# Performance work log

Measured on AMD Instinct MI355X. Metric: run time of the kernel, lower is better.

The kernel has to match this reference:

```python
import jax, jax.numpy as jnp
import numpy as np

V, J, NB, NP = 100000, 24, 10, 207
PARENT = np.array([-1, 0, 0, 0, 1, 2, 3, 4, 5, 6, 7, 8, 9, 9, 9, 12, 13, 14, 16, 17, 18, 19, 20, 21])


def setup_inputs() -> dict:
    key = jax.random.key(0)
    ks = jax.random.split(key, 9)
    return {
        "beta": jax.random.normal(ks[0], (NB,), jnp.float32),
        "pose": jax.random.normal(ks[1], (J, 3), jnp.float32),
        "trans": jax.random.normal(ks[2], (3,), jnp.float32),
        "shapedirs": jax.random.normal(ks[3], (V, 3, NB), jnp.float32),
        "v_template": jax.random.normal(ks[4], (V, 3), jnp.float32),
        "J_regressor": jax.random.uniform(ks[5], (J, V), jnp.float32),
        "posedirs": jax.random.normal(ks[6], (V, 3, NP), jnp.float32),
        "weights": jax.random.uniform(ks[7], (V, J), jnp.float32),
        "faces": jax.random.randint(ks[8], (200000, 3), 0, V, jnp.int32),
    }


def _rodrigues(r):
    # r: [N,3] axis-angle -> [N,3,3] rotation matrices
    theta = jnp.sqrt(jnp.sum(r * r, axis=1, keepdims=True)) + 1e-8  # [N,1]
    rh = r / theta
    c = jnp.cos(theta)[:, :, None]  # [N,1,1]
    s = jnp.sin(theta)[:, :, None]
    z = jnp.zeros_like(rh[:, 0])
    K = jnp.stack([z, -rh[:, 2], rh[:, 1],
                   rh[:, 2], z, -rh[:, 0],
                   -rh[:, 1], rh[:, 0], z], axis=1).reshape(-1, 3, 3)
    outer = rh[:, :, None] * rh[:, None, :]
    I = jnp.eye(3, dtype=r.dtype)
    return c * I + (1.0 - c) * outer + s * K


def _with_zeros(Rt):
    # [3,4] -> [4,4] homogeneous
    bottom = jnp.array([[0.0, 0.0, 0.0, 1.0]], dtype=Rt.dtype)
    return jnp.concatenate([Rt, bottom], axis=0)


def reference(beta, pose, trans, shapedirs, v_template, J_regressor, posedirs, weights, faces):
    # shape blending
    v_shaped = jnp.einsum('vdb,b->vd', shapedirs, beta) + v_template  # [V,3]
    Jts = J_regressor @ v_shaped  # [J,3]
    R = _rodrigues(pose)  # [J,3,3]
    # pose blending: lrotmin = (R[1:] - I).flatten(), length 207
    lrotmin = (R[1:] - jnp.eye(3, dtype=R.dtype)).reshape(-1)
    v_posed = v_shaped + jnp.einsum('vdp,p->vd', posedirs, lrotmin)
    # forward kinematics along the 24-joint chain
    G = [_with_zeros(jnp.concatenate([R[0], Jts[0][:, None]], axis=1))]
    for i in range(1, J):
        p = int(PARENT[i])
        loc = _with_zeros(jnp.concatenate([R[i], (Jts[i] - Jts[p])[:, None]], axis=1))
        G.append(G[p] @ loc)
    stacked = jnp.stack(G, axis=0)  # [J,4,4]
    Jh = jnp.concatenate([Jts, jnp.zeros((J, 1), dtype=Jts.dtype)], axis=1)  # [J,4]
    corr = stacked @ Jh[:, :, None]  # [J,4,1]
    A = stacked - jnp.concatenate([jnp.zeros((J, 4, 3), dtype=stacked.dtype), corr], axis=2)
    # LBS skinning
    T = jnp.einsum('vj,jab->vab', weights, A)  # [V,4,4]
    rest = jnp.concatenate([v_posed, jnp.ones((v_posed.shape[0], 1), dtype=v_posed.dtype)], axis=1)  # [V,4]
    v = jnp.einsum('vab,vb->va', T, rest)[:, :3]
    vertices = v + trans[None, :]
    return vertices, faces
```

## Files before the change

### kernel.cpp

```cpp
#include <hip/hip_runtime.h>

#define V_N 100000
#define J_N 24
#define NB_N 10
#define NP_N 207
#define FLAT_P 621
#define FACE_I 600000
#define CHUNKS 50
#define CHUNK_V 2000
#define K1_BLK 1172
#define F_BLK  587

__device__ __constant__ int PARENT_D[24] = {
    -1, 0, 0, 0, 1, 2, 3, 4, 5, 6, 7, 8, 9, 9, 9, 12, 13, 14, 16, 17, 18, 19, 20, 21
};

__device__ __forceinline__ float wave_sum64(float x) {
    float t;
    t = __int_as_float(__builtin_amdgcn_update_dpp(0, __float_as_int(x), 0x111, 0xf, 0xf, true)); x += t;
    t = __int_as_float(__builtin_amdgcn_update_dpp(0, __float_as_int(x), 0x112, 0xf, 0xf, true)); x += t;
    t = __int_as_float(__builtin_amdgcn_update_dpp(0, __float_as_int(x), 0x114, 0xf, 0xf, true)); x += t;
    t = __int_as_float(__builtin_amdgcn_update_dpp(0, __float_as_int(x), 0x118, 0xf, 0xf, true)); x += t;
    t = __int_as_float(__builtin_amdgcn_update_dpp(0, __float_as_int(x), 0x142, 0xa, 0xf, true)); x += t;
    t = __int_as_float(__builtin_amdgcn_update_dpp(0, __float_as_int(x), 0x143, 0xc, 0xf, true)); x += t;
    return __int_as_float(__builtin_amdgcn_readlane(__float_as_int(x), 63));
}

__global__ __launch_bounds__(256) void kA_shape_faces(const float* __restrict__ shapedirs,
                                                      const float* __restrict__ vtemp,
                                                      const float* __restrict__ beta,
                                                      float* __restrict__ vshaped,
                                                      const int4* __restrict__ faces4,
                                                      float* __restrict__ out) {
    int b = blockIdx.x;
    if (b < K1_BLK) {
        int i = b * 256 + threadIdx.x;
        if (i >= V_N * 3) return;
        const float2* sd2 = reinterpret_cast<const float2*>(shapedirs + (size_t)i * NB_N);
        float2 p0 = sd2[0], p1 = sd2[1], p2 = sd2[2], p3 = sd2[3], p4 = sd2[4];
        float acc = vtemp[i];
        acc += p0.x * beta[0] + p0.y * beta[1];
        acc += p1.x * beta[2] + p1.y * beta[3];
        acc += p2.x * beta[4] + p2.y * beta[5];
        acc += p3.x * beta[6] + p3.y * beta[7];
        acc += p4.x * beta[8] + p4.y * beta[9];
        vshaped[i] = acc;
    } else {
        int i = (b - K1_BLK) * 256 + threadIdx.x;
        if (i < FACE_I / 4) {
            int4 f = faces4[i];
            float4* fdst = reinterpret_cast<float4*>(out + 300000);
            fdst[i] = make_float4((float)f.x, (float)f.y, (float)f.z, (float)f.w);
        }
    }
}

__global__ __launch_bounds__(256) void kB_partial(const float* __restrict__ Jreg,
                                                  const float* __restrict__ vshaped,
                                                  float* __restrict__ partials) {
    int c = blockIdx.x, j = blockIdx.y;
    int t = threadIdx.x;
    const float* row = Jreg + (size_t)j * V_N + (size_t)c * CHUNK_V;
    const float* vs  = vshaped + (size_t)c * CHUNK_V * 3;
    float s0 = 0.f, s1 = 0.f, s2 = 0.f;
    for (int i = t; i < CHUNK_V; i += 256) {
        float w = row[i];
        s0 += w * vs[i * 3 + 0];
        s1 += w * vs[i * 3 + 1];
        s2 += w * vs[i * 3 + 2];
    }
    for (int off = 32; off > 0; off >>= 1) {
        s0 += __shfl_xor(s0, off, 64);
        s1 += __shfl_xor(s1, off, 64);
        s2 += __shfl_xor(s2, off, 64);
    }
    __shared__ float ls[3][4];
    int wv = t >> 6;
    if ((t & 63) == 0) { ls[0][wv] = s0; ls[1][wv] = s1; ls[2][wv] = s2; }
    __syncthreads();
    if (t == 0) {
        float* p = partials + ((size_t)j * CHUNKS + c) * 3;
        p[0] = ls[0][0] + ls[0][1] + ls[0][2] + ls[0][3];
        p[1] = ls[1][0] + ls[1][1] + ls[1][2] + ls[1][3];
        p[2] = ls[2][0] + ls[2][1] + ls[2][2] + ls[2][3];
    }
}

__global__ __launch_bounds__(64) void kC_fk(const float* __restrict__ pose,
                                            const float* __restrict__ partials,
                                            float* __restrict__ ws_lrot,
                                            float* __restrict__ ws_A) {
    __shared__ float R[24][9];
    __shared__ float G[24][12];
    __shared__ float Jts[24][3];
    int t = threadIdx.x;
    for (int u = t; u < 72; u += 64) {
        int j = u / 3, d = u % 3;
        float s = 0.f;
        for (int c = 0; c < CHUNKS; ++c) s += partials[((size_t)j * CHUNKS + c) * 3 + d];
        (&Jts[0][0])[u] = s;
    }
    if (t < 24) {
        float x = pose[t * 3 + 0], y = pose[t * 3 + 1], z = pose[t * 3 + 2];
        float th = sqrtf(x * x + y * y + z * z) + 1e-8f;
        float inv = 1.0f / th;
        float rx = x * inv, ry = y * inv, rz = z * inv;
        float c = cosf(th), s = sinf(th), ic = 1.0f - c;
        R[t][0] = c + ic * rx * rx;      R[t][1] = ic * rx * ry - s * rz;  R[t][2] = ic * rx * rz + s * ry;
        R[t][3] = ic * ry * rx + s * rz; R[t][4] = c + ic * ry * ry;       R[t][5] = ic * ry * rz - s * rx;
        R[t][6] = ic * rz * rx - s * ry; R[t][7] = ic * rz * ry + s * rx;  R[t][8] = c + ic * rz * rz;
    }
    __syncthreads();
    for (int f = t; f < 640; f += 64) {
        float val = 0.0f;
        if (f < FLAT_P) {
            int p = f % NP_N;
            int j = 1 + p / 9;
            int e = p % 9;
            val = R[j][e] - ((e == 0 || e == 4 || e == 8) ? 1.0f : 0.0f);
        }
        ws_lrot[f] = val;
    }
    if (t < 12) {
        int r = t >> 2, c = t & 3;
        G[0][t] = (c < 3) ? R[0][r * 3 + c] : Jts[0][r];
    }
    __syncthreads();
    for (int i = 1; i < J_N; ++i) {
        int p = PARENT_D[i];
        if (t < 12) {
            int r = t >> 2, c = t & 3;
            float sum = (c == 3) ? G[p][r * 4 + 3] : 0.0f;
            #pragma unroll
            for (int k = 0; k < 3; ++k) {
                float loc = (c < 3) ? R[i][k * 3 + c] : (Jts[i][k] - Jts[p][k]);
                sum += G[p][r * 4 + k] * loc;
            }
            G[i][t] = sum;
        }
        __syncthreads();
    }
    for (int u = t; u < 72; u += 64) {
        int j = u / 3, r = u % 3;
        float g0 = G[j][r * 4 + 0], g1 = G[j][r * 4 + 1], g2 = G[j][r * 4 + 2], g3 = G[j][r * 4 + 3];
        float corr = g0 * Jts[j][0] + g1 * Jts[j][1] + g2 * Jts[j][2];
        ws_A[j * 12 + r * 4 + 0] = g0;
        ws_A[j * 12 + r * 4 + 1] = g1;
        ws_A[j * 12 + r * 4 + 2] = g2;
        ws_A[j * 12 + r * 4 + 3] = g3 - corr;
    }
}

__global__ __launch_bounds__(256) void kD_main(const float* __restrict__ posedirs,
                                               const float* __restrict__ weights,
                                               const float* __restrict__ vshaped,
                                               const float* __restrict__ ws_lrot,
                                               const float* __restrict__ ws_A,
                                               const float* __restrict__ trans,
                                               float* __restrict__ out) {
    __shared__ float sL[640];
    __shared__ float sA[288];
    int tid = threadIdx.x;
    for (int i = tid; i < 640; i += 256) sL[i] = ws_lrot[i];
    for (int i = tid; i < 288; i += 256) sA[i] = ws_A[i];
    __syncthreads();

    int lane = tid & 63;
    int v = blockIdx.x * 4 + (tid >> 6);
    if (v >= V_N) return;

    const float* pd = posedirs + (size_t)v * FLAT_P;
    float a0 = 0.f, a1 = 0.f, a2 = 0.f;
    #pragma unroll
    for (int k = 0; k < 10; ++k) {
        int f = lane + k * 64;
        if (f < FLAT_P) {
            float val = pd[f] * sL[f];
            if (f < 207)      a0 += val;
            else if (f < 414) a1 += val;
            else              a2 += val;
        }
    }
    float vp0 = wave_sum64(a0) + vshaped[v * 3 + 0];
    float vp1 = wave_sum64(a1) + vshaped[v * 3 + 1];
    float vp2 = wave_sum64(a2) + vshaped[v * 3 + 2];

    float r0 = 0.f, r1 = 0.f, r2 = 0.f;
    if (lane < J_N) {
        float w = weights[(size_t)v * J_N + lane];
        const float* A = &sA[lane * 12];
        r0 = w * (A[0] * vp0 + A[1] * vp1 + A[2]  * vp2 + A[3]);
        r1 = w * (A[4] * vp0 + A[5] * vp1 + A[6]  * vp2 + A[7]);
        r2 = w * (A[8] * vp0 + A[9] * vp1 + A[10] * vp2 + A[11]);
    }
    float s0 = wave_sum64(r0);
    float s1 = wave_sum64(r1);
    float s2 = wave_sum64(r2);

    if (lane < 3) {
        float res = (lane == 0) ? s0 : (lane == 1) ? s1 : s2;
        out[v * 3 + lane] = res + trans[lane];
    }
}

extern "C" void kernel_launch(void* const* d_in, const int* in_sizes, int n_in,
                              void* d_out, int out_size, void* d_ws, size_t ws_size,
                              hipStream_t stream) {
    const float* beta      = (const float*)d_in[0];
    const float* pose      = (const float*)d_in[1];
    const float* trans     = (const float*)d_in[2];
    const float* shapedirs = (const float*)d_in[3];
    const float* v_template= (const float*)d_in[4];
    const float* J_reg     = (const float*)d_in[5];
    const float* posedirs  = (const float*)d_in[6];
    const float* weights   = (const float*)d_in[7];
    const int*   faces     = (const int*)d_in[8];

    float* out = (float*)d_out;

    float* ws       = (float*)d_ws;
    float* vshaped  = ws;
    float* ws_lrot  = ws + 300080;
    float* ws_A     = ws + 300720;
    float* partials = ws + 301008;

    kA_shape_faces<<<K1_BLK + F_BLK, 256, 0, stream>>>(shapedirs, v_template, beta, vshaped,
                                                       (const int4*)faces, out);
    kB_partial<<<dim3(CHUNKS, J_N), 256, 0, stream>>>(J_reg, vshaped, partials);
    kC_fk<<<1, 64, 0, stream>>>(pose, partials, ws_lrot, ws_A);
    kD_main<<<(V_N + 3) / 4, 256, 0, stream>>>(posedirs, weights, vshaped, ws_lrot, ws_A, trans, out);
}
```

Before: 89.24 us.

## Vectorize posedirs loads with float4 using shifted lrotmin tables per alignment

The main kernel now reads each vertex's 621-float posedirs row with float4 loads aligned to the 16-byte boundary below the row start. It compensates for the row's misalignment by indexing one of four pre-shifted copies of the lrotmin vector, which the FK kernel builds into a larger table. The partials layout is transposed so the Jts reduction reads coalesced, and FK runs with 128 threads. The cost is a bigger shared-memory table per block and reads that spill into neighbouring rows, which rely on the alignment arithmetic being correct.

```diff
diff --git a/kernel.cpp b/kernel.cpp
--- a/kernel.cpp
+++ b/kernel.cpp
@@ -10,6 +10,8 @@
 #define CHUNK_V 2000
 #define K1_BLK 1172
 #define F_BLK  587
+#define TBL_T 192
+#define TBL_N (7 * TBL_T)
 
 __device__ __constant__ int PARENT_D[24] = {
     -1, 0, 0, 0, 1, 2, 3, 4, 5, 6, 7, 8, 9, 9, 9, 12, 13, 14, 16, 17, 18, 19, 20, 21
@@ -79,26 +81,26 @@
     if ((t & 63) == 0) { ls[0][wv] = s0; ls[1][wv] = s1; ls[2][wv] = s2; }
     __syncthreads();
     if (t == 0) {
-        float* p = partials + ((size_t)j * CHUNKS + c) * 3;
+        float* p = partials + (size_t)c * 72 + j * 3;
         p[0] = ls[0][0] + ls[0][1] + ls[0][2] + ls[0][3];
         p[1] = ls[1][0] + ls[1][1] + ls[1][2] + ls[1][3];
         p[2] = ls[2][0] + ls[2][1] + ls[2][2] + ls[2][3];
     }
 }
 
-__global__ __launch_bounds__(64) void kC_fk(const float* __restrict__ pose,
-                                            const float* __restrict__ partials,
-                                            float* __restrict__ ws_lrot,
-                                            float* __restrict__ ws_A) {
+__global__ __launch_bounds__(128) void kC_fk(const float* __restrict__ pose,
+                                             const float* __restrict__ partials,
+                                             float* __restrict__ ws_sd,
+                                             float* __restrict__ ws_A) {
     __shared__ float R[24][9];
     __shared__ float G[24][12];
     __shared__ float Jts[24][3];
     int t = threadIdx.x;
-    for (int u = t; u < 72; u += 64) {
-        int j = u / 3, d = u % 3;
+    if (t < 72) {
         float s = 0.f;
-        for (int c = 0; c < CHUNKS; ++c) s += partials[((size_t)j * CHUNKS + c) * 3 + d];
-        (&Jts[0][0])[u] = s;
+        #pragma unroll
+        for (int c = 0; c < CHUNKS; ++c) s += partials[c * 72 + t];
+        (&Jts[0][0])[t] = s;
     }
     if (t < 24) {
         float x = pose[t * 3 + 0], y = pose[t * 3 + 1], z = pose[t * 3 + 2];
@@ -111,15 +113,18 @@
         R[t][6] = ic * rz * rx - s * ry; R[t][7] = ic * rz * ry + s * rx;  R[t][8] = c + ic * rz * rz;
     }
     __syncthreads();
-    for (int f = t; f < 640; f += 64) {
+    for (int idx = t; idx < TBL_N; idx += 128) {
+        int d  = idx / TBL_T;
+        int tt = idx % TBL_T;
+        int f  = 4 * tt + d - 3;
         float val = 0.0f;
-        if (f < FLAT_P) {
+        if (f >= 0 && f < FLAT_P) {
             int p = f % NP_N;
             int j = 1 + p / 9;
             int e = p % 9;
             val = R[j][e] - ((e == 0 || e == 4 || e == 8) ? 1.0f : 0.0f);
         }
-        ws_lrot[f] = val;
+        ws_sd[idx] = val;
     }
     if (t < 12) {
         int r = t >> 2, c = t & 3;
@@ -140,8 +145,8 @@
         }
         __syncthreads();
     }
-    for (int u = t; u < 72; u += 64) {
-        int j = u / 3, r = u % 3;
+    if (t < 72) {
+        int j = t / 3, r = t % 3;
         float g0 = G[j][r * 4 + 0], g1 = G[j][r * 4 + 1], g2 = G[j][r * 4 + 2], g3 = G[j][r * 4 + 3];
         float corr = g0 * Jts[j][0] + g1 * Jts[j][1] + g2 * Jts[j][2];
         ws_A[j * 12 + r * 4 + 0] = g0;
@@ -154,33 +159,62 @@
 __global__ __launch_bounds__(256) void kD_main(const float* __restrict__ posedirs,
                                                const float* __restrict__ weights,
                                                const float* __restrict__ vshaped,
-                                               const float* __restrict__ ws_lrot,
+                                               const float* __restrict__ ws_sd,
                                                const float* __restrict__ ws_A,
                                                const float* __restrict__ trans,
                                                float* __restrict__ out) {
-    __shared__ float sL[640];
+    __shared__ float sD[TBL_N];
     __shared__ float sA[288];
     int tid = threadIdx.x;
-    for (int i = tid; i < 640; i += 256) sL[i] = ws_lrot[i];
+    for (int i = tid; i < TBL_N; i += 256) sD[i] = ws_sd[i];
     for (int i = tid; i < 288; i += 256) sA[i] = ws_A[i];
     __syncthreads();
 
     int lane = tid & 63;
     int v = blockIdx.x * 4 + (tid >> 6);
-    if (v >= V_N) return;
-
-    const float* pd = posedirs + (size_t)v * FLAT_P;
+
+    int row_start = v * FLAT_P;
+    int bd = row_start & 3;
+    const float4* pbase = reinterpret_cast<const float4*>(posedirs) + (row_start >> 2);
+    int sbase = (3 - bd) * TBL_T;
+
     float a0 = 0.f, a1 = 0.f, a2 = 0.f;
-    #pragma unroll
-    for (int k = 0; k < 10; ++k) {
-        int f = lane + k * 64;
-        if (f < FLAT_P) {
-            float val = pd[f] * sL[f];
-            if (f < 207)      a0 += val;
-            else if (f < 414) a1 += val;
-            else              a2 += val;
-        }
-    }
+    {
+        int t = lane;
+        float4 p = pbase[t];
+        const float* pf = reinterpret_cast<const float*>(&p);
+        int f0 = 4 * t - bd;
+        #pragma unroll
+        for (int e = 0; e < 4; ++e) {
+            float val = pf[e] * sD[sbase + e * TBL_T + t];
+            bool c = (f0 + e) < 207;
+            a0 += c ? val : 0.0f;
+            a1 += c ? 0.0f : val;
+        }
+    }
+    {
+        int t = lane + 64;
+        float4 p = pbase[t];
+        const float* pf = reinterpret_cast<const float*>(&p);
+        int f0 = 4 * t - bd;
+        #pragma unroll
+        for (int e = 0; e < 4; ++e) {
+            float val = pf[e] * sD[sbase + e * TBL_T + t];
+            bool c = (f0 + e) < 414;
+            a1 += c ? val : 0.0f;
+            a2 += c ? 0.0f : val;
+        }
+    }
+    if (lane < 28) {
+        int t = lane + 128;
+        float4 p = pbase[t];
+        const float* pf = reinterpret_cast<const float*>(&p);
+        #pragma unroll
+        for (int e = 0; e < 4; ++e) {
+            a2 += pf[e] * sD[sbase + e * TBL_T + t];
+        }
+    }
+
     float vp0 = wave_sum64(a0) + vshaped[v * 3 + 0];
     float vp1 = wave_sum64(a1) + vshaped[v * 3 + 1];
     float vp2 = wave_sum64(a2) + vshaped[v * 3 + 2];
@@ -220,13 +254,13 @@
 
     float* ws       = (float*)d_ws;
     float* vshaped  = ws;
-    float* ws_lrot  = ws + 300080;
-    float* ws_A     = ws + 300720;
-    float* partials = ws + 301008;
+    float* ws_sd    = ws + 300080;
+    float* ws_A     = ws + 301504;
+    float* partials = ws + 301808;
 
     kA_shape_faces<<<K1_BLK + F_BLK, 256, 0, stream>>>(shapedirs, v_template, beta, vshaped,
                                                        (const int4*)faces, out);
     kB_partial<<<dim3(CHUNKS, J_N), 256, 0, stream>>>(J_reg, vshaped, partials);
-    kC_fk<<<1, 64, 0, stream>>>(pose, partials, ws_lrot, ws_A);
-    kD_main<<<(V_N + 3) / 4, 256, 0, stream>>>(posedirs, weights, vshaped, ws_lrot, ws_A, trans, out);
-}
+    kC_fk<<<1, 128, 0, stream>>>(pose, partials, ws_sd, ws_A);
+    kD_main<<<V_N / 4, 256, 0, stream>>>(posedirs, weights, vshaped, ws_sd, ws_A, trans, out);
+}
```

Result: slower. 98.95 us (+10.9%).
